# Performance work log

Measured on AMD Instinct MI355X. Metric: run time of the kernel, lower is better.

The kernel has to match this reference:

```python
import jax, jax.numpy as jnp
import numpy as np


def _construct_A_B(H, W):
    # Per-pixel epipolar coefficient tensors, shapes [2, 3, H, W]
    y, x = jnp.meshgrid(jnp.arange(H, dtype=jnp.float32),
                        jnp.arange(W, dtype=jnp.float32), indexing='ij')
    ones = jnp.ones_like(x)
    zeros = jnp.zeros_like(x)
    A = jnp.stack([-ones, zeros, x,
                   zeros, -ones, y], axis=0).reshape(2, 3, H, W)
    B = jnp.stack([x * y, -(x ** 2 + 1.0), y,
                   y ** 2 + 1.0, -x * y, -x], axis=0).reshape(2, 3, H, W)
    return A, B


def setup_inputs() -> dict:
    key = jax.random.key(0)
    k1, k2, k3 = jax.random.split(key, 3)
    Bn, H, W = 16, 480, 640
    pose = jax.random.normal(k1, (Bn, 6), dtype=jnp.float32)
    grad_dirs = jax.random.normal(k2, (Bn, 2, H, W), dtype=jnp.float32)
    normal_flow = jax.random.normal(k3, (Bn, 2, H, W), dtype=jnp.float32)
    return {"pose": pose, "grad_dirs": grad_dirs, "normal_flow": normal_flow}


def reference(pose, grad_dirs, normal_flow):
    # pose: [B, 6] (V = translation, Omega = rotation); grad_dirs/normal_flow: [B, 2, H, W]
    Bn, _, H, W = grad_dirs.shape
    V, Omega = pose[:, :3], pose[:, 3:]
    A, Bm = _construct_A_B(H, W)
    # Contract 3 coefficient channels against the 3-vectors (vectorized over batch)
    AV = jnp.einsum('dchw,bc->bdhw', A, V)       # [B, 2, H, W]
    BW = jnp.einsum('dchw,bc->bdhw', Bm, Omega)  # [B, 2, H, W]
    # rho per pixel: (g . Av) * (sum_d nf - g . Bw)
    rho = (grad_dirs * AV).sum(axis=1) * (normal_flow.sum(axis=1) - (grad_dirs * BW).sum(axis=1))
    # per-image mean of GELU(-rho), averaged over batch == global mean
    return jax.nn.gelu(-rho, approximate=False).mean()
```

## Files before the change

### kernel.cpp

```cpp
#include <hip/hip_runtime.h>
#include <math.h>

#define BN 16
#define H  480
#define W  640
#define HW (H * W)
#define QUADS_PER_IMG (HW / 4)
#define TOTAL_QUADS (BN * QUADS_PER_IMG)
#define INV_N (1.0f / (float)(BN * HW))

__global__ __launch_bounds__(256) void cheirality_kernel(
    const float* __restrict__ pose,
    const float* __restrict__ grad,
    const float* __restrict__ nf,
    float* __restrict__ out)
{
    __shared__ float sp[BN * 6];
    if (threadIdx.x < BN * 6) sp[threadIdx.x] = pose[threadIdx.x];
    __syncthreads();

    float local = 0.0f;

    const int stride = gridDim.x * blockDim.x;
    for (int q = blockIdx.x * blockDim.x + threadIdx.x; q < TOTAL_QUADS; q += stride) {
        const int b = q / QUADS_PER_IMG;
        const int r = q - b * QUADS_PER_IMG;
        const int p = r << 2;
        const int row = p / W;
        const int col = p - row * W;

        const float fy  = (float)row;
        const float fy2p1 = fy * fy + 1.0f;

        const size_t base = (size_t)b * (2 * HW) + p;
        const float4 g0 = *(const float4*)(grad + base);
        const float4 g1 = *(const float4*)(grad + base + HW);
        const float4 n0 = *(const float4*)(nf   + base);
        const float4 n1 = *(const float4*)(nf   + base + HW);

        const float V0 = sp[b * 6 + 0];
        const float V1 = sp[b * 6 + 1];
        const float V2 = sp[b * 6 + 2];
        const float W0 = sp[b * 6 + 3];
        const float W1 = sp[b * 6 + 4];
        const float W2 = sp[b * 6 + 5];

        const float g0v[4] = {g0.x, g0.y, g0.z, g0.w};
        const float g1v[4] = {g1.x, g1.y, g1.z, g1.w};
        const float n0v[4] = {n0.x, n0.y, n0.z, n0.w};
        const float n1v[4] = {n1.x, n1.y, n1.z, n1.w};

        #pragma unroll
        for (int i = 0; i < 4; ++i) {
            const float fx = (float)(col + i);
            const float AV0 = fmaf(fx, V2, -V0);
            const float AV1 = fmaf(fy, V2, -V1);
            const float xy = fx * fy;
            const float BW0 = fmaf(xy, W0, fmaf(-(fx * fx + 1.0f), W1, fy * W2));
            const float BW1 = fmaf(fy2p1, W0, fmaf(-xy, W1, -fx * W2));

            const float s1 = fmaf(g0v[i], AV0, g1v[i] * AV1);
            const float s3 = fmaf(g0v[i], BW0, g1v[i] * BW1);
            const float rho = s1 * ((n0v[i] + n1v[i]) - s3);

            const float z = -rho;
            const float g = 0.5f * z * (1.0f + erff(z * 0.70710678118654752f));
            local += g;
        }
    }

    #pragma unroll
    for (int off = 32; off > 0; off >>= 1)
        local += __shfl_down(local, off, 64);

    __shared__ float waveSums[4];
    const int lane = threadIdx.x & 63;
    const int wid  = threadIdx.x >> 6;
    if (lane == 0) waveSums[wid] = local;
    __syncthreads();

    if (threadIdx.x == 0) {
        const float s = waveSums[0] + waveSums[1] + waveSums[2] + waveSums[3];
        atomicAdd(out, s * INV_N);
    }
}

extern "C" void kernel_launch(void* const* d_in, const int* in_sizes, int n_in,
                              void* d_out, int out_size, void* d_ws, size_t ws_size,
                              hipStream_t stream) {
    const float* pose = (const float*)d_in[0];
    const float* grad = (const float*)d_in[1];
    const float* nf   = (const float*)d_in[2];
    float* out = (float*)d_out;

    hipMemsetAsync(out, 0, sizeof(float), stream);

    const int blocks = 2400;
    cheirality_kernel<<<blocks, 256, 0, stream>>>(pose, grad, nf, out);
}
```

Measured before the change: 127.2 us.

## Fix per-thread pixel mapping, prefetch across images, use two-stage reduction

Each thread now owns one fixed pixel quad and iterates over four images with a fixed stride. This lets the per-pixel coordinate terms be computed once and the next image's loads be issued before the current one is computed. The global atomic and memset are replaced by per-block partial sums in workspace plus a single-block reduce kernel. The trade is an extra kernel launch and a grid size hardcoded to the problem shape.

Result: faster. 104.3 us (-18.0%).

```diff
diff --git a/kernel.cpp b/kernel.cpp
--- a/kernel.cpp
+++ b/kernel.cpp
@@ -9,63 +9,86 @@
 #define TOTAL_QUADS (BN * QUADS_PER_IMG)
 #define INV_N (1.0f / (float)(BN * HW))
 
-__global__ __launch_bounds__(256) void cheirality_kernel(
+#define THREADS 256
+#define BLOCKS  1200
+#define ITERS   4
+
+__global__ __launch_bounds__(THREADS) void cheirality_main(
     const float* __restrict__ pose,
     const float* __restrict__ grad,
     const float* __restrict__ nf,
-    float* __restrict__ out)
+    float* __restrict__ partial)
 {
     __shared__ float sp[BN * 6];
     if (threadIdx.x < BN * 6) sp[threadIdx.x] = pose[threadIdx.x];
     __syncthreads();
 
+    const int tid0 = blockIdx.x * THREADS + threadIdx.x;
+    const int b0   = tid0 / QUADS_PER_IMG;
+    const int r    = tid0 - b0 * QUADS_PER_IMG;
+    const int p    = r << 2;
+    const int row  = p / W;
+    const int col  = p - row * W;
+
+    const float fy    = (float)row;
+    const float fy2p1 = fy * fy + 1.0f;
+    float fxv[4], xyv[4], x2p1[4];
+    #pragma unroll
+    for (int i = 0; i < 4; ++i) {
+        const float fx = (float)(col + i);
+        fxv[i]  = fx;
+        xyv[i]  = fx * fy;
+        x2p1[i] = fx * fx + 1.0f;
+    }
+
     float local = 0.0f;
 
-    const int stride = gridDim.x * blockDim.x;
-    for (int q = blockIdx.x * blockDim.x + threadIdx.x; q < TOTAL_QUADS; q += stride) {
-        const int b = q / QUADS_PER_IMG;
-        const int r = q - b * QUADS_PER_IMG;
-        const int p = r << 2;
-        const int row = p / W;
-        const int col = p - row * W;
+    int b = b0;
+    size_t base = (size_t)b * (2 * HW) + p;
+    float4 g0 = *(const float4*)(grad + base);
+    float4 g1 = *(const float4*)(grad + base + HW);
+    float4 n0 = *(const float4*)(nf   + base);
+    float4 n1 = *(const float4*)(nf   + base + HW);
 
-        const float fy  = (float)row;
-        const float fy2p1 = fy * fy + 1.0f;
+    #pragma unroll
+    for (int it = 0; it < ITERS; ++it) {
+        const float4 cg0 = g0, cg1 = g1, cn0 = n0, cn1 = n1;
+        const int cb = b;
+        if (it + 1 < ITERS) {
+            b += 4;
+            base = (size_t)b * (2 * HW) + p;
+            g0 = *(const float4*)(grad + base);
+            g1 = *(const float4*)(grad + base + HW);
+            n0 = *(const float4*)(nf   + base);
+            n1 = *(const float4*)(nf   + base + HW);
+        }
 
-        const size_t base = (size_t)b * (2 * HW) + p;
-        const float4 g0 = *(const float4*)(grad + base);
-        const float4 g1 = *(const float4*)(grad + base + HW);
-        const float4 n0 = *(const float4*)(nf   + base);
-        const float4 n1 = *(const float4*)(nf   + base + HW);
+        const float V0 = sp[cb * 6 + 0];
+        const float V1 = sp[cb * 6 + 1];
+        const float V2 = sp[cb * 6 + 2];
+        const float W0 = sp[cb * 6 + 3];
+        const float W1 = sp[cb * 6 + 4];
+        const float W2 = sp[cb * 6 + 5];
 
-        const float V0 = sp[b * 6 + 0];
-        const float V1 = sp[b * 6 + 1];
-        const float V2 = sp[b * 6 + 2];
-        const float W0 = sp[b * 6 + 3];
-        const float W1 = sp[b * 6 + 4];
-        const float W2 = sp[b * 6 + 5];
+        const float AV1 = fmaf(fy, V2, -V1);
 
-        const float g0v[4] = {g0.x, g0.y, g0.z, g0.w};
-        const float g1v[4] = {g1.x, g1.y, g1.z, g1.w};
-        const float n0v[4] = {n0.x, n0.y, n0.z, n0.w};
-        const float n1v[4] = {n1.x, n1.y, n1.z, n1.w};
+        const float g0a[4] = {cg0.x, cg0.y, cg0.z, cg0.w};
+        const float g1a[4] = {cg1.x, cg1.y, cg1.z, cg1.w};
+        const float n0a[4] = {cn0.x, cn0.y, cn0.z, cn0.w};
+        const float n1a[4] = {cn1.x, cn1.y, cn1.z, cn1.w};
 
         #pragma unroll
         for (int i = 0; i < 4; ++i) {
-            const float fx = (float)(col + i);
-            const float AV0 = fmaf(fx, V2, -V0);
-            const float AV1 = fmaf(fy, V2, -V1);
-            const float xy = fx * fy;
-            const float BW0 = fmaf(xy, W0, fmaf(-(fx * fx + 1.0f), W1, fy * W2));
-            const float BW1 = fmaf(fy2p1, W0, fmaf(-xy, W1, -fx * W2));
+            const float AV0 = fmaf(fxv[i], V2, -V0);
+            const float BW0 = fmaf(xyv[i], W0, fmaf(-x2p1[i], W1, fy * W2));
+            const float BW1 = fmaf(fy2p1, W0, fmaf(-xyv[i], W1, -fxv[i] * W2));
 
-            const float s1 = fmaf(g0v[i], AV0, g1v[i] * AV1);
-            const float s3 = fmaf(g0v[i], BW0, g1v[i] * BW1);
-            const float rho = s1 * ((n0v[i] + n1v[i]) - s3);
+            const float s1  = fmaf(g0a[i], AV0, g1a[i] * AV1);
+            const float s3  = fmaf(g0a[i], BW0, g1a[i] * BW1);
+            const float rho = s1 * ((n0a[i] + n1a[i]) - s3);
 
             const float z = -rho;
-            const float g = 0.5f * z * (1.0f + erff(z * 0.70710678118654752f));
-            local += g;
+            local += 0.5f * z * (1.0f + erff(z * 0.70710678118654752f));
         }
     }
 
@@ -73,16 +96,35 @@
     for (int off = 32; off > 0; off >>= 1)
         local += __shfl_down(local, off, 64);
 
-    __shared__ float waveSums[4];
+    __shared__ float waveSums[THREADS / 64];
     const int lane = threadIdx.x & 63;
     const int wid  = threadIdx.x >> 6;
     if (lane == 0) waveSums[wid] = local;
     __syncthreads();
 
-    if (threadIdx.x == 0) {
-        const float s = waveSums[0] + waveSums[1] + waveSums[2] + waveSums[3];
-        atomicAdd(out, s * INV_N);
-    }
+    if (threadIdx.x == 0)
+        partial[blockIdx.x] = waveSums[0] + waveSums[1] + waveSums[2] + waveSums[3];
+}
+
+__global__ __launch_bounds__(256) void cheirality_reduce(
+    const float* __restrict__ partial, float* __restrict__ out)
+{
+    float v = 0.0f;
+    for (int i = threadIdx.x; i < BLOCKS; i += 256)
+        v += partial[i];
+
+    #pragma unroll
+    for (int off = 32; off > 0; off >>= 1)
+        v += __shfl_down(v, off, 64);
+
+    __shared__ float waveSums[4];
+    const int lane = threadIdx.x & 63;
+    const int wid  = threadIdx.x >> 6;
+    if (lane == 0) waveSums[wid] = v;
+    __syncthreads();
+
+    if (threadIdx.x == 0)
+        out[0] = (waveSums[0] + waveSums[1] + waveSums[2] + waveSums[3]) * INV_N;
 }
 
 extern "C" void kernel_launch(void* const* d_in, const int* in_sizes, int n_in,
@@ -91,10 +133,9 @@
     const float* pose = (const float*)d_in[0];
     const float* grad = (const float*)d_in[1];
     const float* nf   = (const float*)d_in[2];
-    float* out = (float*)d_out;
+    float* out     = (float*)d_out;
+    float* partial = (float*)d_ws;
 
-    hipMemsetAsync(out, 0, sizeof(float), stream);
-
-    const int blocks = 2400;
-    cheirality_kernel<<<blocks, 256, 0, stream>>>(pose, grad, nf, out);
+    cheirality_main<<<BLOCKS, THREADS, 0, stream>>>(pose, grad, nf, partial);
+    cheirality_reduce<<<1, 256, 0, stream>>>(partial, out);
 }
```
